# Optimization experiments

Measured on AMD Instinct MI355X. Metric: run time of the kernel, lower is better.

## Reference

```python
import jax, jax.numpy as jnp
import numpy as np

B, L, D = 2, 1024, 768
NH, HD = 12, 64
NL = 6
MLP = 3072
THETA = 10000.0


def _rope(pos, dim, theta):
    # pos: (L,) float -> (L, dim//2, 2, 2) rotation matrices (FLUX rope)
    omega = 1.0 / (theta ** (jnp.arange(0, dim, 2, dtype=jnp.float32) / dim))
    out = pos[:, None] * omega  # (L, dim//2)
    cos, sin = jnp.cos(out), jnp.sin(out)
    return jnp.stack([jnp.stack([cos, -sin], -1), jnp.stack([sin, cos], -1)], -2)


def _build_pe(seq_len, pe_dim):
    # 2D spatial ids: axis0 = x (fast), axis1 = y (slow); axes_dim = [pe_dim//2, pe_dim//2]
    h = w = int(seq_len ** 0.5)
    y_ids = jnp.repeat(jnp.arange(h, dtype=jnp.float32), w)
    x_ids = jnp.tile(jnp.arange(w, dtype=jnp.float32), h)
    half = pe_dim // 2
    pe = jnp.concatenate([_rope(x_ids, half, THETA), _rope(y_ids, half, THETA)], axis=-3)
    return pe[None, None]  # (1, 1, L, pe_dim//2, 2, 2)


def _apply_rope(x, pe):
    # x: (B, H, L, HD)
    xs = x.reshape(x.shape[:-1] + (-1, 1, 2))
    out = pe[..., 0] * xs[..., 0] + pe[..., 1] * xs[..., 1]
    return out.reshape(x.shape)


def _rmsnorm(x, scale):
    return x * jax.lax.rsqrt(jnp.mean(x * x, axis=-1, keepdims=True) + 1e-6) * scale


def _layernorm(x, g, b):
    m = jnp.mean(x, axis=-1, keepdims=True)
    v = jnp.var(x, axis=-1, keepdims=True)
    return (x - m) * jax.lax.rsqrt(v + 1e-5) * g + b


def _forward(spatial_features, density_weights, condition_embeddings,
             spatial_w, spatial_b, cond_w, cond_b,
             ln1_g, ln1_b, qkv_w, q_scale, k_scale, proj_w, proj_b,
             dscale, dbias, ln2_g, ln2_b, mlp_w1, mlp_b1, mlp_w2, mlp_b2,
             out_w, out_b):
    Bsz, Ls, Ds = spatial_features.shape
    x = spatial_features @ spatial_w + spatial_b
    x = x + (condition_embeddings @ cond_w + cond_b)[:, None, :]
    pe = _build_pe(Ls, HD)
    dflat = density_weights.reshape(Bsz, 1, Ls)  # H*W == L, no interpolation
    attn_scale = HD ** -0.5
    for i in range(NL):
        h = _layernorm(x, ln1_g[i], ln1_b[i])
        qkv = (h @ qkv_w[i]).reshape(Bsz, Ls, 3, NH, HD).transpose(2, 0, 3, 1, 4)
        q, k, v = qkv[0], qkv[1], qkv[2]
        q = _rmsnorm(q, q_scale[i])
        k = _rmsnorm(k, k_scale[i])
        q = _apply_rope(q, pe)
        k = _apply_rope(k, pe)
        scores = jnp.einsum('bhld,bhmd->bhlm', q, k) * attn_scale
        scores = scores + (dscale[i] * dflat[..., None] + dbias[i])  # (B,1,L,1) bcast
        attn = jax.nn.softmax(scores, axis=-1)
        o = jnp.einsum('bhlm,bhmd->bhld', attn, v)
        o = o.transpose(0, 2, 1, 3).reshape(Bsz, Ls, Ds)
        x = x + o @ proj_w[i] + proj_b[i]
        h2 = _layernorm(x, ln2_g[i], ln2_b[i])
        x = x + jax.nn.gelu(h2 @ mlp_w1[i] + mlp_b1[i], approximate=False) @ mlp_w2[i] + mlp_b2[i]
    return x @ out_w + out_b


def setup_inputs() -> dict:
    key = jax.random.key(0)
    ks = jax.random.split(key, 16)
    s = 0.02
    inp = {
        'spatial_features': jax.random.normal(ks[0], (B, L, D), jnp.float32),
        'density_weights': jax.random.uniform(ks[1], (B, 32, 32), jnp.float32),
        'condition_embeddings': jax.random.normal(ks[2], (B, 1536), jnp.float32),
        'spatial_w': jax.random.normal(ks[3], (D, D), jnp.float32) * s,
        'spatial_b': jnp.zeros((D,), jnp.float32),
        'cond_w': jax.random.normal(ks[4], (1536, D), jnp.float32) * s,
        'cond_b': jnp.zeros((D,), jnp.float32),
        'ln1_g': jnp.ones((NL, D), jnp.float32),
        'ln1_b': jnp.zeros((NL, D), jnp.float32),
        'qkv_w': jax.random.normal(ks[5], (NL, D, 3 * D), jnp.float32) * s,
        'q_scale': jnp.ones((NL, HD), jnp.float32),
        'k_scale': jnp.ones((NL, HD), jnp.float32),
        'proj_w': jax.random.normal(ks[6], (NL, D, D), jnp.float32) * s,
        'proj_b': jnp.zeros((NL, D), jnp.float32),
        'dscale': jnp.ones((NL,), jnp.float32),
        'dbias': jnp.zeros((NL,), jnp.float32),
        'ln2_g': jnp.ones((NL, D), jnp.float32),
        'ln2_b': jnp.zeros((NL, D), jnp.float32),
        'mlp_w1': jax.random.normal(ks[7], (NL, D, MLP), jnp.float32) * s,
        'mlp_b1': jnp.zeros((NL, MLP), jnp.float32),
        'mlp_w2': jax.random.normal(ks[8], (NL, MLP, D), jnp.float32) * s,
        'mlp_b2': jnp.zeros((NL, D), jnp.float32),
        'out_w': jax.random.normal(ks[9], (D, D), jnp.float32) * s,
        'out_b': jnp.zeros((D,), jnp.float32),
    }
    return inp


def reference(spatial_features, density_weights, condition_embeddings,
              spatial_w, spatial_b, cond_w, cond_b,
              ln1_g, ln1_b, qkv_w, q_scale, k_scale, proj_w, proj_b,
              dscale, dbias, ln2_g, ln2_b, mlp_w1, mlp_b1, mlp_w2, mlp_b2,
              out_w, out_b):
    return _forward(spatial_features, density_weights, condition_embeddings,
                    spatial_w, spatial_b, cond_w, cond_b,
                    ln1_g, ln1_b, qkv_w, q_scale, k_scale, proj_w, proj_b,
                    dscale, dbias, ln2_g, ln2_b, mlp_w1, mlp_b1, mlp_w2, mlp_b2,
                    out_w, out_b)
```

## Files before the change

kernel.cpp:

```cpp
#include <hip/hip_runtime.h>
#include <hip/hip_bf16.h>
#include <cstdint>
#include <cstddef>

typedef unsigned short u16;
using short8  = __attribute__((ext_vector_type(8))) short;
using floatx4 = __attribute__((ext_vector_type(4))) float;

typedef __attribute__((address_space(1))) void gvoid;
typedef __attribute__((address_space(3))) void svoid;

__device__ __forceinline__ u16 f2bf(float f) {
  __hip_bfloat16 h = __float2bfloat16(f);
  return __builtin_bit_cast(u16, h);
}

__device__ __forceinline__ floatx4 mfma16(short8 a, short8 b, floatx4 c) {
  return __builtin_amdgcn_mfma_f32_16x16x32_bf16(a, b, c, 0, 0, 0);
}

__device__ __forceinline__ void glds16(const u16* g, u16* l) {
  __builtin_amdgcn_global_load_lds((gvoid*)g, (svoid*)l, 16, 0, 0);
}

__global__ void pe_kernel(float* __restrict__ pet) {
  int t = blockIdx.x * 256 + threadIdx.x;
  if (t >= 32768) return;
  int l = t >> 5, j = t & 31;
  float pos   = (j < 16) ? (float)(l & 31) : (float)(l >> 5);
  float omega = powf(10000.f, -(float)(j & 15) / 16.f);
  float a = pos * omega;
  pet[2 * t]     = cosf(a);
  pet[2 * t + 1] = sinf(a);
}

__global__ __launch_bounds__(256) void twt_kernel(const float* __restrict__ in,
                                                  u16* __restrict__ out, int K, int N) {
  size_t lofs = (size_t)blockIdx.z * K * N;
  in  += lofs;
  out += lofs;
  __shared__ float tile[32][33];
  int bx = blockIdx.x;
  int by = blockIdx.y;
  int tx = threadIdx.x & 31, ty = threadIdx.x >> 5;
  #pragma unroll
  for (int p = 0; p < 4; p++) {
    int k = by * 32 + ty + p * 8;
    tile[ty + p * 8][tx] = in[(size_t)k * N + bx * 32 + tx];
  }
  __syncthreads();
  #pragma unroll
  for (int p = 0; p < 4; p++) {
    int n = bx * 32 + ty + p * 8;
    out[(size_t)n * K + by * 32 + tx] = f2bf(tile[tx][ty + p * 8]);
  }
}

__global__ void cvt_kernel(const float* __restrict__ in, u16* __restrict__ out, int n) {
  int i = blockIdx.x * 256 + threadIdx.x;
  if (i < n) out[i] = f2bf(in[i]);
}

__global__ __launch_bounds__(256) void condp_kernel(const float* __restrict__ ce,
                                                    const float* __restrict__ w,
                                                    float* __restrict__ partial) {
  int d = blockIdx.x * 256 + threadIdx.x;
  int c = blockIdx.y;
  #pragma unroll
  for (int b = 0; b < 2; b++) {
    float acc = 0.f;
    #pragma unroll 4
    for (int k = c * 96; k < c * 96 + 96; k++) acc += ce[b * 1536 + k] * w[(size_t)k * 768 + d];
    partial[(size_t)(c * 2 + b) * 768 + d] = acc;
  }
}

__global__ __launch_bounds__(256) void condr_kernel(const float* __restrict__ partial,
                                                    const float* __restrict__ bias,
                                                    float* __restrict__ out) {
  int t = blockIdx.x * 256 + threadIdx.x;
  int b = t / 768, d = t % 768;
  float acc = bias[d];
  #pragma unroll
  for (int c = 0; c < 16; c++) acc += partial[(size_t)(c * 2 + b) * 768 + d];
  out[b * 768 + d] = acc;
}

__global__ __launch_bounds__(256) void ln_kernel(const float* __restrict__ x,
                                                 const float* __restrict__ g,
                                                 const float* __restrict__ b,
                                                 u16* __restrict__ out) {
  int row = blockIdx.x;
  const float* xr = x + (size_t)row * 768;
  int t = threadIdx.x;
  float v0 = xr[t], v1 = xr[t + 256], v2 = xr[t + 512];
  float s = v0 + v1 + v2, s2 = v0 * v0 + v1 * v1 + v2 * v2;
  #pragma unroll
  for (int o = 32; o >= 1; o >>= 1) { s += __shfl_xor(s, o); s2 += __shfl_xor(s2, o); }
  __shared__ float red[8];
  int w = t >> 6, lane = t & 63;
  if (lane == 0) { red[w] = s; red[4 + w] = s2; }
  __syncthreads();
  s  = red[0] + red[1] + red[2] + red[3];
  s2 = red[4] + red[5] + red[6] + red[7];
  float mean = s * (1.f / 768.f);
  float var  = s2 * (1.f / 768.f) - mean * mean;
  float rstd = rsqrtf(var + 1e-5f);
  u16* orow = out + (size_t)row * 768;
  orow[t]       = f2bf((v0 - mean) * rstd * g[t] + b[t]);
  orow[t + 256] = f2bf((v1 - mean) * rstd * g[t + 256] + b[t + 256]);
  orow[t + 512] = f2bf((v2 - mean) * rstd * g[t + 512] + b[t + 512]);
}

__global__ __launch_bounds__(256) void ropeq_kernel(const float* __restrict__ qkv,
                                                    const float* __restrict__ qs,
                                                    const float* __restrict__ ks,
                                                    const float* __restrict__ pet,
                                                    u16* __restrict__ qb, u16* __restrict__ kb) {
  int gid = blockIdx.x * 4 + (threadIdx.x >> 6);
  int lane = threadIdx.x & 63;
  int h = gid % 12, bl = gid / 12;
  int l = bl & 1023, b = bl >> 10;
  const float* qp = qkv + ((size_t)(b * 1024 + l) * 3 + 0) * 768 + h * 64;
  const float* kp = qp + 768;
  float q = qp[lane], k = kp[lane];
  float sq = q * q, sk = k * k;
  #pragma unroll
  for (int o = 1; o < 64; o <<= 1) { sq += __shfl_xor(sq, o); sk += __shfl_xor(sk, o); }
  q *= rsqrtf(sq * (1.f / 64.f) + 1e-6f) * qs[lane];
  k *= rsqrtf(sk * (1.f / 64.f) + 1e-6f) * ks[lane];
  int j = lane >> 1;
  float c = pet[(l * 32 + j) * 2], s = pet[(l * 32 + j) * 2 + 1];
  float qo = __shfl_xor(q, 1), ko = __shfl_xor(k, 1);
  float qr = (lane & 1) ? (s * qo + c * q) : (c * q - s * qo);
  float kr = (lane & 1) ? (s * ko + c * k) : (c * k - s * ko);
  int bh = b * 12 + h;
  qb[((size_t)bh * 1024 + l) * 64 + lane] = f2bf(qr * 0.125f);
  kb[((size_t)bh * 1024 + l) * 64 + lane] = f2bf(kr);
}

__global__ __launch_bounds__(256) void vtrans_kernel(const float* __restrict__ qkv,
                                                     u16* __restrict__ vt) {
  int lt = blockIdx.x, bh = blockIdx.y;
  int b = bh / 12, h = bh % 12;
  __shared__ float tile[64][65];
  int t = threadIdx.x, c = t & 63, r0 = t >> 6;
  #pragma unroll
  for (int p = 0; p < 16; p++) {
    int lr = p * 4 + r0;
    tile[lr][c] = qkv[((size_t)(b * 1024 + lt * 64 + lr) * 3 + 2) * 768 + h * 64 + c];
  }
  __syncthreads();
  #pragma unroll
  for (int p = 0; p < 16; p++) {
    int d = p * 4 + r0;
    vt[((size_t)bh * 64 + d) * 1024 + lt * 64 + c] = f2bf(tile[c][d]);
  }
}

__global__ __launch_bounds__(256) void attn_split(const u16* __restrict__ qb,
                                                  const u16* __restrict__ kbuf,
                                                  const u16* __restrict__ vt,
                                                  float* __restrict__ po,
                                                  float* __restrict__ pl) {
  const int qt = blockIdx.x, bh = blockIdx.y, sp = blockIdx.z;
  const int lane = threadIdx.x & 63, w = threadIdx.x >> 6;
  const int quad = lane >> 4, l16 = lane & 15;
  __shared__ __align__(16) u16 Ks[128 * 64];
  __shared__ __align__(16) u16 Vs[64 * 128];
  __shared__ __align__(16) u16 Ps[4][16 * 136];
  const u16* Q  = qb   + (size_t)bh * 1024 * 64;
  const u16* Kp = kbuf + (size_t)bh * 1024 * 64;
  const u16* Vp = vt   + (size_t)bh * 64 * 1024;
  const int qrow0 = qt * 64 + w * 16;
  short8 aq0, aq1;
  {
    const u16* qp = Q + (size_t)(qrow0 + l16) * 64 + quad * 8;
    aq0 = *(const short8*)qp;
    aq1 = *(const short8*)(qp + 32);
  }
  floatx4 accO[4];
  #pragma unroll
  for (int i = 0; i < 4; i++) accO[i] = (floatx4){0.f, 0.f, 0.f, 0.f};
  float lsum[4] = {0.f, 0.f, 0.f, 0.f};

  const int krow_in = (lane >> 3);
  const int kchunk  = lane & 7;
  const int vrow_in = (lane >> 4);
  const int vchunk  = lane & 15;

  for (int nt = 0; nt < 4; ++nt) {
    const int kb0 = sp * 512 + nt * 128;
    __syncthreads();
    #pragma unroll
    for (int j = 0; j < 4; j++) {
      int r = w * 32 + j * 8 + krow_in;
      int g = kchunk ^ (r & 7);
      glds16(Kp + (size_t)(kb0 + r) * 64 + g * 8, Ks + (w * 32 + j * 8) * 64);
    }
    #pragma unroll
    for (int j = 0; j < 4; j++) {
      int r = w * 16 + j * 4 + vrow_in;
      int g = vchunk ^ (r & 15);
      glds16(Vp + (size_t)r * 1024 + kb0 + g * 8, Vs + (w * 16 + j * 4) * 128);
    }
    __syncthreads();

    floatx4 s[8];
    #pragma unroll
    for (int n = 0; n < 8; n++) {
      int row = n * 16 + l16;
      int c0 = quad ^ (l16 & 7);
      short8 b0 = *(const short8*)&Ks[row * 64 + c0 * 8];
      short8 b1 = *(const short8*)&Ks[row * 64 + (c0 ^ 4) * 8];
      floatx4 z = (floatx4){0.f, 0.f, 0.f, 0.f};
      z = mfma16(aq0, b0, z);
      s[n] = mfma16(aq1, b1, z);
    }
    #pragma unroll
    for (int n = 0; n < 8; n++) {
      #pragma unroll
      for (int r = 0; r < 4; r++) {
        float pv = __expf(s[n][r] - 8.f);
        lsum[r] += pv;
        Ps[w][(quad * 4 + r) * 136 + n * 16 + l16] = f2bf(pv);
      }
    }
    #pragma unroll
    for (int kt = 0; kt < 4; kt++) {
      short8 ap = *(const short8*)&Ps[w][l16 * 136 + kt * 32 + quad * 8];
      #pragma unroll
      for (int dt = 0; dt < 4; dt++) {
        int vrow = dt * 16 + l16;
        int c = (kt * 4 + quad) ^ l16;
        short8 bv = *(const short8*)&Vs[vrow * 128 + c * 8];
        accO[dt] = mfma16(ap, bv, accO[dt]);
      }
    }
  }
  #pragma unroll
  for (int r = 0; r < 4; r++) {
    #pragma unroll
    for (int o = 1; o < 16; o <<= 1) lsum[r] += __shfl_xor(lsum[r], o);
  }
  const size_t sb = (size_t)(sp * 24 + bh) * 1024;
  #pragma unroll
  for (int r = 0; r < 4; r++) {
    int lr = qrow0 + quad * 4 + r;
    if (l16 == 0) pl[sb + lr] = lsum[r];
    #pragma unroll
    for (int dt = 0; dt < 4; dt++)
      po[(sb + lr) * 64 + dt * 16 + l16] = accO[dt][r];
  }
}

__global__ __launch_bounds__(256) void attn_comb(const float* __restrict__ po,
                                                 const float* __restrict__ pl,
                                                 u16* __restrict__ obuf) {
  int w = threadIdx.x >> 6, lane = threadIdx.x & 63;
  int gr = blockIdx.x * 4 + w;
  int bh = gr >> 10, l = gr & 1023;
  float num = 0.f, den = 0.f;
  #pragma unroll
  for (int s = 0; s < 2; s++) {
    num += po[((size_t)(s * 24 + bh) * 1024 + l) * 64 + lane];
    den += pl[(size_t)(s * 24 + bh) * 1024 + l];
  }
  int b = bh / 12, h = bh % 12;
  obuf[((size_t)(b * 1024 + l)) * 768 + h * 64 + lane] = f2bf(num / den);
}

template <int EPI, int BN>
__global__ __launch_bounds__(256) void gemm_bt(const u16* __restrict__ A,
                                               const u16* __restrict__ Bt,
                                               const float* __restrict__ bias,
                                               const float* extra,
                                               float* Cf, u16* Cb, int M, int N, int K) {
  constexpr int ROWS = 64 + BN;
  constexpr int NTW  = BN / 32;
  constexpr int PC   = ROWS / 64;
  __shared__ __align__(16) u16 S[ROWS * 32];
  u16* As = S;
  u16* Bs = S + 64 * 32;
  const int t = threadIdx.x;
  const int lane = t & 63, w = t >> 6;
  const int quad = lane >> 4, l16 = lane & 15;
  const int m0 = blockIdx.y * 64, n0 = blockIdx.x * BN;
  const int wm = (w >> 1) * 32, wn = (w & 1) * (BN / 2);
  floatx4 acc[2][NTW];
  #pragma unroll
  for (int i = 0; i < 2; i++)
    #pragma unroll
    for (int j = 0; j < NTW; j++) acc[i][j] = (floatx4){0.f, 0.f, 0.f, 0.f};

  const u16* gp[PC];
  u16* lp[PC];
  #pragma unroll
  for (int j = 0; j < PC; j++) {
    int c = w * PC + j;
    int r = lane >> 2;
    const u16* base = (c < 4) ? (A + (size_t)(m0 + c * 16 + r) * K)
                              : (Bt + (size_t)(n0 + (c - 4) * 16 + r) * K);
    gp[j] = base + (lane & 3) * 8;
    lp[j] = S + c * 16 * 32;
  }

  for (int k0 = 0; k0 < K; k0 += 32) {
    #pragma unroll
    for (int j = 0; j < PC; j++) glds16(gp[j] + k0, lp[j]);
    __syncthreads();
    short8 af[2], bfr[NTW];
    #pragma unroll
    for (int mt = 0; mt < 2; mt++)
      af[mt] = *(const short8*)&As[(wm + mt * 16 + l16) * 32 + quad * 8];
    #pragma unroll
    for (int nt = 0; nt < NTW; nt++)
      bfr[nt] = *(const short8*)&Bs[(wn + nt * 16 + l16) * 32 + quad * 8];
    #pragma unroll
    for (int mt = 0; mt < 2; mt++)
      #pragma unroll
      for (int nt = 0; nt < NTW; nt++)
        acc[mt][nt] = mfma16(af[mt], bfr[nt], acc[mt][nt]);
    __syncthreads();
  }

  #pragma unroll
  for (int mt = 0; mt < 2; mt++) {
    #pragma unroll
    for (int nt = 0; nt < NTW; nt++) {
      int col = n0 + wn + nt * 16 + l16;
      float bcol = bias ? bias[col] : 0.f;
      #pragma unroll
      for (int r = 0; r < 4; r++) {
        int row = m0 + wm + mt * 16 + quad * 4 + r;
        float v = acc[mt][nt][r] + bcol;
        if (EPI == 1) v += extra[(row >> 10) * N + col];
        if (EPI == 2) v += extra[(size_t)row * N + col];
        if (EPI == 3) v = 0.5f * v * (1.f + erff(v * 0.70710678118654752f));
        if (Cf) Cf[(size_t)row * N + col] = v;
        if (Cb) Cb[(size_t)row * N + col] = f2bf(v);
      }
    }
  }
}

extern "C" void kernel_launch(void* const* d_in, const int* in_sizes, int n_in,
                              void* d_out, int out_size, void* d_ws, size_t ws_size,
                              hipStream_t stream) {
  const float* sf   = (const float*)d_in[0];
  const float* ce   = (const float*)d_in[2];
  const float* sw   = (const float*)d_in[3];
  const float* sb   = (const float*)d_in[4];
  const float* cw   = (const float*)d_in[5];
  const float* cb   = (const float*)d_in[6];
  const float* ln1g = (const float*)d_in[7];
  const float* ln1b = (const float*)d_in[8];
  const float* qkvw = (const float*)d_in[9];
  const float* qsc  = (const float*)d_in[10];
  const float* ksc  = (const float*)d_in[11];
  const float* pw   = (const float*)d_in[12];
  const float* pb   = (const float*)d_in[13];
  const float* ln2g = (const float*)d_in[16];
  const float* ln2b = (const float*)d_in[17];
  const float* w1   = (const float*)d_in[18];
  const float* b1   = (const float*)d_in[19];
  const float* w2   = (const float*)d_in[20];
  const float* b2   = (const float*)d_in[21];
  const float* ow   = (const float*)d_in[22];
  const float* ob   = (const float*)d_in[23];

  char* p = (char*)d_ws;
  auto alloc = [&](size_t bytes) { char* r = p; p += (bytes + 255) & ~(size_t)255; return r; };
  float* pet  = (float*)alloc((size_t)1024 * 32 * 2 * 4);
  u16* swT    = (u16*)alloc((size_t)768 * 768 * 2);
  u16* owT    = (u16*)alloc((size_t)768 * 768 * 2);
  u16* qkvT   = (u16*)alloc((size_t)6 * 2304 * 768 * 2);
  u16* pwT    = (u16*)alloc((size_t)6 * 768 * 768 * 2);
  u16* w1T    = (u16*)alloc((size_t)6 * 3072 * 768 * 2);
  u16* w2T    = (u16*)alloc((size_t)6 * 768 * 3072 * 2);
  u16* sfb    = (u16*)alloc((size_t)2048 * 768 * 2);
  float* cpar = (float*)alloc((size_t)32 * 768 * 4);
  float* cond = (float*)alloc((size_t)2 * 768 * 4);
  float* x    = (float*)alloc((size_t)2048 * 768 * 4);
  u16* xb     = (u16*)alloc((size_t)2048 * 768 * 2);
  u16* h      = (u16*)alloc((size_t)2048 * 768 * 2);
  float* qkv  = (float*)alloc((size_t)2048 * 2304 * 4);
  u16* qbuf   = (u16*)alloc((size_t)2048 * 768 * 2);
  u16* kbuf   = (u16*)alloc((size_t)2048 * 768 * 2);
  u16* vtb    = (u16*)alloc((size_t)2048 * 768 * 2);
  u16* obuf   = (u16*)alloc((size_t)2048 * 768 * 2);
  u16* gbuf   = (u16*)alloc((size_t)2048 * 3072 * 2);
  float* po   = (float*)alloc((size_t)2 * 24 * 1024 * 64 * 4);
  float* pl   = (float*)alloc((size_t)2 * 24 * 1024 * 4);

  pe_kernel<<<128, 256, 0, stream>>>(pet);
  twt_kernel<<<dim3(24, 24, 1), 256, 0, stream>>>(sw, swT, 768, 768);
  twt_kernel<<<dim3(24, 24, 1), 256, 0, stream>>>(ow, owT, 768, 768);
  twt_kernel<<<dim3(72, 24, 6), 256, 0, stream>>>(qkvw, qkvT, 768, 2304);
  twt_kernel<<<dim3(24, 24, 6), 256, 0, stream>>>(pw, pwT, 768, 768);
  twt_kernel<<<dim3(96, 24, 6), 256, 0, stream>>>(w1, w1T, 768, 3072);
  twt_kernel<<<dim3(24, 96, 6), 256, 0, stream>>>(w2, w2T, 3072, 768);
  cvt_kernel<<<(2048 * 768) / 256, 256, 0, stream>>>(sf, sfb, 2048 * 768);
  condp_kernel<<<dim3(3, 16), 256, 0, stream>>>(ce, cw, cpar);
  condr_kernel<<<6, 256, 0, stream>>>(cpar, cb, cond);

  gemm_bt<1, 64><<<dim3(12, 32), 256, 0, stream>>>(sfb, swT, sb, cond, x, nullptr, 2048, 768, 768);

  for (int i = 0; i < 6; i++) {
    ln_kernel<<<2048, 256, 0, stream>>>(x, ln1g + i * 768, ln1b + i * 768, h);
    gemm_bt<0, 128><<<dim3(18, 32), 256, 0, stream>>>(h, qkvT + (size_t)i * 2304 * 768,
                                                      nullptr, nullptr, qkv, nullptr, 2048, 2304, 768);
    ropeq_kernel<<<6144, 256, 0, stream>>>(qkv, qsc + i * 64, ksc + i * 64, pet, qbuf, kbuf);
    vtrans_kernel<<<dim3(16, 24), 256, 0, stream>>>(qkv, vtb);
    attn_split<<<dim3(16, 24, 2), 256, 0, stream>>>(qbuf, kbuf, vtb, po, pl);
    attn_comb<<<6144, 256, 0, stream>>>(po, pl, obuf);
    gemm_bt<2, 64><<<dim3(12, 32), 256, 0, stream>>>(obuf, pwT + (size_t)i * 768 * 768,
                                                     pb + i * 768, x, x, xb, 2048, 768, 768);
    ln_kernel<<<2048, 256, 0, stream>>>(x, ln2g + i * 768, ln2b + i * 768, h);
    gemm_bt<3, 128><<<dim3(24, 32), 256, 0, stream>>>(h, w1T + (size_t)i * 3072 * 768,
                                                      b1 + i * 3072, nullptr, nullptr, gbuf, 2048, 3072, 768);
    gemm_bt<2, 64><<<dim3(12, 32), 256, 0, stream>>>(gbuf, w2T + (size_t)i * 768 * 3072,
                                                     b2 + i * 768, x, x, xb, 2048, 768, 3072);
  }
  gemm_bt<0, 64><<<dim3(12, 32), 256, 0, stream>>>(xb, owT, ob, nullptr, (float*)d_out, nullptr,
                                                   2048, 768, 768);
}
```

Before: 1.198 ms.

## Double-buffer GEMM tiles via register staging with K=64 steps and padded LDS

Replaces the direct global-to-LDS loads, which used a single buffer and two barriers per 32-wide K step, with register-staged global loads feeding two padded LDS buffers (row stride 72). Each stage now covers 64 of K, so the next tiles are prefetched into registers while MFMAs run on the current buffer. This aims to hide global-load latency, halve the number of barriers per K, and reduce LDS bank conflicts through padding. In exchange it uses more registers and LDS, which can lower occupancy, and it assumes K is a multiple of 128.

```diff
diff --git a/kernel.cpp b/kernel.cpp
--- a/kernel.cpp
+++ b/kernel.cpp
@@ -277,11 +277,10 @@
                                                const float* extra,
                                                float* Cf, u16* Cb, int M, int N, int K) {
   constexpr int ROWS = 64 + BN;
+  constexpr int LDW  = 72;
+  constexpr int NCH  = ROWS * 8 / 256;
   constexpr int NTW  = BN / 32;
-  constexpr int PC   = ROWS / 64;
-  __shared__ __align__(16) u16 S[ROWS * 32];
-  u16* As = S;
-  u16* Bs = S + 64 * 32;
+  __shared__ __align__(16) u16 S[2][ROWS * LDW];
   const int t = threadIdx.x;
   const int lane = t & 63, w = t >> 6;
   const int quad = lane >> 4, l16 = lane & 15;
@@ -293,34 +292,65 @@
     #pragma unroll
     for (int j = 0; j < NTW; j++) acc[i][j] = (floatx4){0.f, 0.f, 0.f, 0.f};
 
-  const u16* gp[PC];
-  u16* lp[PC];
-  #pragma unroll
-  for (int j = 0; j < PC; j++) {
-    int c = w * PC + j;
-    int r = lane >> 2;
-    const u16* base = (c < 4) ? (A + (size_t)(m0 + c * 16 + r) * K)
-                              : (Bt + (size_t)(n0 + (c - 4) * 16 + r) * K);
-    gp[j] = base + (lane & 3) * 8;
-    lp[j] = S + c * 16 * 32;
-  }
-
-  for (int k0 = 0; k0 < K; k0 += 32) {
-    #pragma unroll
-    for (int j = 0; j < PC; j++) glds16(gp[j] + k0, lp[j]);
+  const u16* gsrc[NCH];
+  int laddr[NCH];
+  #pragma unroll
+  for (int j = 0; j < NCH; j++) {
+    int idx = j * 256 + t;
+    int row = idx >> 3, c = idx & 7;
+    const u16* base = (row < 64) ? (A + (size_t)(m0 + row) * K)
+                                 : (Bt + (size_t)(n0 + row - 64) * K);
+    gsrc[j] = base + c * 8;
+    laddr[j] = row * LDW + c * 8;
+  }
+  short8 stg0[NCH], stg1[NCH];
+
+  const int NIT = K / 64;
+
+  #pragma unroll
+  for (int j = 0; j < NCH; j++) stg0[j] = *(const short8*)(gsrc[j]);
+  #pragma unroll
+  for (int j = 0; j < NCH; j++) stg1[j] = *(const short8*)(gsrc[j] + 64);
+  #pragma unroll
+  for (int j = 0; j < NCH; j++) *(short8*)&S[0][laddr[j]] = stg0[j];
+  __syncthreads();
+
+  auto compute = [&](int buf) {
+    #pragma unroll
+    for (int kk = 0; kk < 2; kk++) {
+      short8 af[2], bfr[NTW];
+      #pragma unroll
+      for (int mt = 0; mt < 2; mt++)
+        af[mt] = *(const short8*)&S[buf][(wm + mt * 16 + l16) * LDW + kk * 32 + quad * 8];
+      #pragma unroll
+      for (int nt = 0; nt < NTW; nt++)
+        bfr[nt] = *(const short8*)&S[buf][(64 + wn + nt * 16 + l16) * LDW + kk * 32 + quad * 8];
+      #pragma unroll
+      for (int mt = 0; mt < 2; mt++)
+        #pragma unroll
+        for (int nt = 0; nt < NTW; nt++)
+          acc[mt][nt] = mfma16(af[mt], bfr[nt], acc[mt][nt]);
+    }
+  };
+
+  for (int it = 0; it < NIT; it += 2) {
+    if (it + 2 < NIT) {
+      #pragma unroll
+      for (int j = 0; j < NCH; j++) stg0[j] = *(const short8*)(gsrc[j] + (it + 2) * 64);
+    }
+    compute(0);
+    #pragma unroll
+    for (int j = 0; j < NCH; j++) *(short8*)&S[1][laddr[j]] = stg1[j];
     __syncthreads();
-    short8 af[2], bfr[NTW];
-    #pragma unroll
-    for (int mt = 0; mt < 2; mt++)
-      af[mt] = *(const short8*)&As[(wm + mt * 16 + l16) * 32 + quad * 8];
-    #pragma unroll
-    for (int nt = 0; nt < NTW; nt++)
-      bfr[nt] = *(const short8*)&Bs[(wn + nt * 16 + l16) * 32 + quad * 8];
-    #pragma unroll
-    for (int mt = 0; mt < 2; mt++)
-      #pragma unroll
-      for (int nt = 0; nt < NTW; nt++)
-        acc[mt][nt] = mfma16(af[mt], bfr[nt], acc[mt][nt]);
+    if (it + 3 < NIT) {
+      #pragma unroll
+      for (int j = 0; j < NCH; j++) stg1[j] = *(const short8*)(gsrc[j] + (it + 3) * 64);
+    }
+    compute(1);
+    if (it + 2 < NIT) {
+      #pragma unroll
+      for (int j = 0; j < NCH; j++) *(short8*)&S[0][laddr[j]] = stg0[j];
+    }
     __syncthreads();
   }
 
```

Result: faster. 1.120 ms (-6.5%).
